# Kernel tuning notes

Hardware: AMD Instinct MI355X
Metric: run time of the kernel (lower is better)

The kernel has to match this reference:

```python
import jax, jax.numpy as jnp
import numpy as np

N_NODES = 50000
N_EDGES = 800000
NUM_GRAPHS = 256
IN_FEAT = 64
REL_DIM = 32
HID = 128
NUM_RELS = 32
NUM_BASES = 8
NUM_LAYERS = 2


def setup_inputs() -> dict:
    key = jax.random.key(0)
    ks = jax.random.split(key, 24)
    s = 0.05
    inp = {
        'feat': jax.random.normal(ks[0], (N_NODES, IN_FEAT), jnp.float32),
        'query_rel': jax.random.randint(ks[1], (N_NODES,), 0, NUM_RELS),
        'src': jax.random.randint(ks[2], (N_EDGES,), 0, N_NODES),
        'dst': jax.random.randint(ks[3], (N_EDGES,), 0, N_NODES),
        'etypes': jax.random.randint(ks[4], (N_EDGES,), 0, NUM_RELS),
        'graph_id': jnp.sort(jax.random.randint(ks[5], (N_NODES,), 0, NUM_GRAPHS)),
        # parameters
        'rel_emb': jax.random.normal(ks[6], (NUM_RELS, REL_DIM), jnp.float32) * s,
        'W_in': jax.random.normal(ks[7], (IN_FEAT + REL_DIM, HID), jnp.float32) * s,
        'b_in': jnp.zeros((HID,), jnp.float32),
        'V': jax.random.normal(ks[8], (NUM_LAYERS, NUM_BASES, HID, HID), jnp.float32) * s,
        'comp': jax.random.normal(ks[9], (NUM_LAYERS, NUM_RELS, NUM_BASES), jnp.float32) * s,
        'W_loop': jax.random.normal(ks[10], (NUM_LAYERS, HID, HID), jnp.float32) * s,
        'b_loop': jnp.zeros((NUM_LAYERS, HID), jnp.float32),
        'W_attn': jax.random.normal(ks[11], (HID + REL_DIM, HID), jnp.float32) * s,
        'b_attn': jnp.zeros((HID,), jnp.float32),
        'w_score_attn': jax.random.normal(ks[12], (HID,), jnp.float32) * s,
        'b_score_attn': jnp.zeros((), jnp.float32),
        'w_out': jax.random.normal(ks[13], (HID,), jnp.float32) * s,
        'b_out': jnp.zeros((), jnp.float32),
    }
    return inp


def _forward(feat, rel_emb, W_in, b_in, V, comp, W_loop, b_loop,
             W_attn, b_attn, w_score_attn, b_score_attn, w_out, b_out,
             query_rel, src, dst, etypes, graph_id):
    N = feat.shape[0]
    er = rel_emb[query_rel]                                   # [N, R]
    h = jax.nn.relu(jnp.concatenate([feat, er], -1) @ W_in + b_in)  # [N, H]
    for l in range(NUM_LAYERS):
        # basis-first: transform all nodes by every basis, then gather+mix per edge
        t = jnp.einsum('nd,bde->bne', h, V[l])                # [B, N, H]
        c = comp[l][etypes]                                   # [E, B]
        msg = jnp.zeros((src.shape[0], HID), h.dtype)
        for b in range(NUM_BASES):                            # fixed small loop
            msg = msg + c[:, b:b + 1] * t[b][src]
        agg = jax.ops.segment_sum(msg, dst, num_segments=N)   # scatter-add to dst
        h = jax.nn.relu(agg + h @ W_loop[l] + b_loop[l])      # self-loop + bias
    # per-graph attention-weighted softmax pooling (segment softmax)
    a = jnp.tanh(jnp.concatenate([h, er], -1) @ W_attn + b_attn) @ w_score_attn + b_score_attn  # [N]
    m = jax.ops.segment_max(a, graph_id, num_segments=NUM_GRAPHS)
    ex = jnp.exp(a - m[graph_id])
    ssum = jax.ops.segment_sum(ex, graph_id, num_segments=NUM_GRAPHS)
    alpha = ex / ssum[graph_id]                               # [N]
    z = jax.ops.segment_sum(h * alpha[:, None], graph_id, num_segments=NUM_GRAPHS)  # [G, H]
    return z @ w_out + b_out                                  # [G]


def reference(feat, query_rel, src, dst, etypes, graph_id,
              rel_emb, W_in, b_in, V, comp, W_loop, b_loop,
              W_attn, b_attn, w_score_attn, b_score_attn, w_out, b_out):
    return _forward(feat, rel_emb, W_in, b_in, V, comp, W_loop, b_loop,
                    W_attn, b_attn, w_score_attn, b_score_attn, w_out, b_out,
                    query_rel, src, dst, etypes, graph_id)
```

## Files before the change

kernel.cpp:

```cpp
#include <hip/hip_runtime.h>
#include <hip/hip_fp16.h>

#define N_NODES   50000
#define N_EDGES   800000
#define NUM_GRAPHS 256
#define IN_FEAT   64
#define REL_DIM   32
#define HID       128
#define NUM_RELS  32
#define NUM_BASES 8
#define NUM_LAYERS 2

#define NBUCK 196
#define PBLK  512
#define CHUNK 1563
#define OFFN  (NBUCK * PBLK)
#define SC2_BLKS (OFFN / 256)

typedef __attribute__((ext_vector_type(8))) _Float16 f16x8;
typedef __attribute__((ext_vector_type(4))) float f32x4;
typedef __attribute__((ext_vector_type(2))) float f32x2;

__device__ __forceinline__ void gld_lds16(void* lds, const void* g) {
    __builtin_amdgcn_global_load_lds(
        (const __attribute__((address_space(1))) unsigned int*)g,
        (__attribute__((address_space(3))) unsigned int*)lds, 16, 0, 0);
}

__global__ void __launch_bounds__(256) k_bhist(const int* __restrict__ dst,
                                               int* __restrict__ off) {
    __shared__ int hist[NBUCK];
    int t = threadIdx.x;
    if (t < NBUCK) hist[t] = 0;
    __syncthreads();
    int base = blockIdx.x * CHUNK;
    for (int i = t; i < CHUNK; i += 256) {
        int e = base + i;
        if (e < N_EDGES) atomicAdd(&hist[dst[e] >> 8], 1);
    }
    __syncthreads();
    if (t < NBUCK) off[t * PBLK + blockIdx.x] = hist[t];
}

__global__ void __launch_bounds__(256) k_scan2_a(int* __restrict__ off,
                                                 int* __restrict__ bsum) {
    __shared__ int s[256];
    int t = threadIdx.x;
    int idx = blockIdx.x * 256 + t;
    int v = off[idx];
    s[t] = v;
    __syncthreads();
    for (int o = 1; o < 256; o <<= 1) {
        int u = (t >= o) ? s[t - o] : 0;
        __syncthreads();
        s[t] += u;
        __syncthreads();
    }
    off[idx] = s[t] - v;
    if (t == 255) bsum[blockIdx.x] = s[255];
}

__global__ void __launch_bounds__(512) k_scan2_b(int* __restrict__ bsum,
                                                 int* __restrict__ boff) {
    __shared__ int s[512];
    int t = threadIdx.x;
    int v = (t < SC2_BLKS) ? bsum[t] : 0;
    s[t] = v;
    __syncthreads();
    for (int o = 1; o < 512; o <<= 1) {
        int u = (t >= o) ? s[t - o] : 0;
        __syncthreads();
        s[t] += u;
        __syncthreads();
    }
    if (t < SC2_BLKS) boff[t] = s[t] - v;
}

__global__ void __launch_bounds__(256) k_scan2_c(int* __restrict__ off,
                                                 const int* __restrict__ boff) {
    int idx = blockIdx.x * 256 + threadIdx.x;
    off[idx] += boff[blockIdx.x];
}

__global__ void __launch_bounds__(256) k_bscatter(
    const int* __restrict__ src, const int* __restrict__ dst,
    const int* __restrict__ ety, const int* __restrict__ off,
    int* __restrict__ tmp) {
    __shared__ int cur[NBUCK];
    int t = threadIdx.x;
    if (t < NBUCK) cur[t] = off[t * PBLK + blockIdx.x];
    __syncthreads();
    int base = blockIdx.x * CHUNK;
    for (int i = t; i < CHUNK; i += 256) {
        int e = base + i;
        if (e < N_EDGES) {
            int d = dst[e];
            int pos = atomicAdd(&cur[d >> 8], 1);
            tmp[pos] = ((d & 255) << 21) | (src[e] << 5) | ety[e];
        }
    }
}

__global__ void __launch_bounds__(256) k_bsort(
    const int* __restrict__ off, const int* __restrict__ tmp,
    int* __restrict__ edge_p, int* __restrict__ row_start) {
    int b = blockIdx.x, t = threadIdx.x;
    int eb = off[b * PBLK];
    int ee = (b == NBUCK - 1) ? N_EDGES : off[(b + 1) * PBLK];
    __shared__ int cnt[256];
    __shared__ int cur[256];
    cnt[t] = 0;
    __syncthreads();
    for (int i = eb + t; i < ee; i += 256)
        atomicAdd(&cnt[(tmp[i] >> 21) & 255], 1);
    __syncthreads();
    int v = cnt[t];
    __shared__ int s[256];
    s[t] = v;
    __syncthreads();
    for (int o = 1; o < 256; o <<= 1) {
        int u = (t >= o) ? s[t - o] : 0;
        __syncthreads();
        s[t] += u;
        __syncthreads();
    }
    int excl = s[t] - v;
    cur[t] = eb + excl;
    int node = b * 256 + t;
    if (node < N_NODES) row_start[node] = eb + excl;
    if (b == NBUCK - 1 && t == 0) row_start[N_NODES] = N_EDGES;
    __syncthreads();
    for (int i = eb + t; i < ee; i += 256) {
        int x = tmp[i];
        int pos = atomicAdd(&cur[(x >> 21) & 255], 1);
        edge_p[pos] = x & 0x1FFFFF;
    }
}

__global__ void __launch_bounds__(128) k_input(
    const float* __restrict__ feat, const int* __restrict__ qrel,
    const float* __restrict__ rel_emb, const float* __restrict__ Wi,
    const float* __restrict__ bi, unsigned short* __restrict__ h16,
    float* __restrict__ er) {
    int n0 = blockIdx.x * 16;
    int j = threadIdx.x;
    int u = j >> 3, q = j & 7;
    __shared__ float xT[96][16];
    {
        const float4* f4 = (const float4*)(feat + (size_t)(n0 + u) * IN_FEAT);
        float4 a = f4[q], b = f4[q + 8];
        xT[4 * q + 0][u] = a.x; xT[4 * q + 1][u] = a.y;
        xT[4 * q + 2][u] = a.z; xT[4 * q + 3][u] = a.w;
        xT[32 + 4 * q + 0][u] = b.x; xT[32 + 4 * q + 1][u] = b.y;
        xT[32 + 4 * q + 2][u] = b.z; xT[32 + 4 * q + 3][u] = b.w;
        int qr = qrel[n0 + u];
        float4 e4 = ((const float4*)(rel_emb + (size_t)qr * REL_DIM))[q];
        xT[64 + 4 * q + 0][u] = e4.x; xT[64 + 4 * q + 1][u] = e4.y;
        xT[64 + 4 * q + 2][u] = e4.z; xT[64 + 4 * q + 3][u] = e4.w;
        ((float4*)(er + (size_t)(n0 + u) * REL_DIM))[q] = e4;
    }
    __syncthreads();
    float bj = bi[j];
    float acc[16];
#pragma unroll
    for (int k = 0; k < 16; k++) acc[k] = bj;
    for (int d = 0; d < 96; d++) {
        float w = Wi[d * HID + j];
        float4 x0 = *(const float4*)&xT[d][0];
        float4 x1 = *(const float4*)&xT[d][4];
        float4 x2 = *(const float4*)&xT[d][8];
        float4 x3 = *(const float4*)&xT[d][12];
        acc[0]  = fmaf(x0.x, w, acc[0]);  acc[1]  = fmaf(x0.y, w, acc[1]);
        acc[2]  = fmaf(x0.z, w, acc[2]);  acc[3]  = fmaf(x0.w, w, acc[3]);
        acc[4]  = fmaf(x1.x, w, acc[4]);  acc[5]  = fmaf(x1.y, w, acc[5]);
        acc[6]  = fmaf(x1.z, w, acc[6]);  acc[7]  = fmaf(x1.w, w, acc[7]);
        acc[8]  = fmaf(x2.x, w, acc[8]);  acc[9]  = fmaf(x2.y, w, acc[9]);
        acc[10] = fmaf(x2.z, w, acc[10]); acc[11] = fmaf(x2.w, w, acc[11]);
        acc[12] = fmaf(x3.x, w, acc[12]); acc[13] = fmaf(x3.y, w, acc[13]);
        acc[14] = fmaf(x3.z, w, acc[14]); acc[15] = fmaf(x3.w, w, acc[15]);
    }
#pragma unroll
    for (int k = 0; k < 16; k++) {
        float v = fmaxf(acc[k], 0.f);
        __half hv = __float2half(v);
        h16[(size_t)(n0 + k) * HID + j] = __builtin_bit_cast(unsigned short, hv);
    }
}

__global__ void __launch_bounds__(256) k_mix2(
    const unsigned short* __restrict__ h16, const float* __restrict__ comp_l,
    const int* __restrict__ row_start, const int* __restrict__ edge_p,
    unsigned short* __restrict__ Gf, int c0, int nc) {
    __shared__ f32x2 cs2[NUM_RELS * NUM_BASES];
    if (threadIdx.x < NUM_RELS * NUM_BASES) {
        float c = comp_l[threadIdx.x];
        cs2[threadIdx.x] = (f32x2){c, c};
    }
    __syncthreads();
    int wave = threadIdx.x >> 6, lane = threadIdx.x & 63;
    int n = c0 + blockIdx.x * 4 + wave;
    if (n >= c0 + nc) return;
    int e0 = row_start[n], e1 = row_start[n + 1];
    f32x2 acc[NUM_BASES] = {};
    int e = e0;
    for (; e + 8 <= e1; e += 8) {
        int p0 = edge_p[e],     p1 = edge_p[e + 1], p2 = edge_p[e + 2], p3 = edge_p[e + 3];
        int p4 = edge_p[e + 4], p5 = edge_p[e + 5], p6 = edge_p[e + 6], p7 = edge_p[e + 7];
        unsigned u0 = ((const unsigned*)(h16 + (size_t)(p0 >> 5) * HID))[lane];
        unsigned u1 = ((const unsigned*)(h16 + (size_t)(p1 >> 5) * HID))[lane];
        unsigned u2 = ((const unsigned*)(h16 + (size_t)(p2 >> 5) * HID))[lane];
        unsigned u3 = ((const unsigned*)(h16 + (size_t)(p3 >> 5) * HID))[lane];
        unsigned u4 = ((const unsigned*)(h16 + (size_t)(p4 >> 5) * HID))[lane];
        unsigned u5 = ((const unsigned*)(h16 + (size_t)(p5 >> 5) * HID))[lane];
        unsigned u6 = ((const unsigned*)(h16 + (size_t)(p6 >> 5) * HID))[lane];
        unsigned u7 = ((const unsigned*)(h16 + (size_t)(p7 >> 5) * HID))[lane];
        const f32x2* c0p = &cs2[(p0 & 31) * NUM_BASES];
        const f32x2* c1p = &cs2[(p1 & 31) * NUM_BASES];
        const f32x2* c2p = &cs2[(p2 & 31) * NUM_BASES];
        const f32x2* c3p = &cs2[(p3 & 31) * NUM_BASES];
        const f32x2* c4p = &cs2[(p4 & 31) * NUM_BASES];
        const f32x2* c5p = &cs2[(p5 & 31) * NUM_BASES];
        const f32x2* c6p = &cs2[(p6 & 31) * NUM_BASES];
        const f32x2* c7p = &cs2[(p7 & 31) * NUM_BASES];
        float2 t0 = __half22float2(__builtin_bit_cast(__half2, u0));
        float2 t1 = __half22float2(__builtin_bit_cast(__half2, u1));
        float2 t2 = __half22float2(__builtin_bit_cast(__half2, u2));
        float2 t3 = __half22float2(__builtin_bit_cast(__half2, u3));
        float2 t4 = __half22float2(__builtin_bit_cast(__half2, u4));
        float2 t5 = __half22float2(__builtin_bit_cast(__half2, u5));
        float2 t6 = __half22float2(__builtin_bit_cast(__half2, u6));
        float2 t7 = __half22float2(__builtin_bit_cast(__half2, u7));
        f32x2 v0 = {t0.x, t0.y}, v1 = {t1.x, t1.y}, v2 = {t2.x, t2.y}, v3 = {t3.x, t3.y};
        f32x2 v4 = {t4.x, t4.y}, v5 = {t5.x, t5.y}, v6 = {t6.x, t6.y}, v7 = {t7.x, t7.y};
#pragma unroll
        for (int b = 0; b < NUM_BASES; b++) {
            acc[b] += c0p[b] * v0;
            acc[b] += c1p[b] * v1;
            acc[b] += c2p[b] * v2;
            acc[b] += c3p[b] * v3;
            acc[b] += c4p[b] * v4;
            acc[b] += c5p[b] * v5;
            acc[b] += c6p[b] * v6;
            acc[b] += c7p[b] * v7;
        }
    }
    for (; e < e1; e++) {
        int se = edge_p[e];
        const f32x2* cp = &cs2[(se & 31) * NUM_BASES];
        unsigned u = ((const unsigned*)(h16 + (size_t)(se >> 5) * HID))[lane];
        float2 tv = __half22float2(__builtin_bit_cast(__half2, u));
        f32x2 v = {tv.x, tv.y};
#pragma unroll
        for (int b = 0; b < NUM_BASES; b++) acc[b] += cp[b] * v;
    }
    size_t base = (size_t)(n - c0) * 1024 + 2 * lane;
#pragma unroll
    for (int b = 0; b < NUM_BASES; b++) {
        __half2 g2 = __floats2half2_rn(acc[b][0], acc[b][1]);
        *(unsigned*)&Gf[base + b * 128] = __builtin_bit_cast(unsigned, g2);
    }
}

__global__ void k_bfrag(const float* __restrict__ V, const float* __restrict__ W_loop,
                        unsigned short* __restrict__ Bf) {
    int idx = blockIdx.x * 256 + threadIdx.x;
    if (idx >= NUM_LAYERS * 36 * 8 * 64) return;
    int lane = idx & 63;
    int t = (idx >> 6) & 7;
    int s = (idx >> 9) % 36;
    int l = (idx >> 9) / 36;
    int col = t * 16 + (lane & 15);
    int kbase = s * 32 + (lane >> 4) * 8;
    unsigned short* o = Bf + (size_t)idx * 8;
#pragma unroll
    for (int j = 0; j < 8; j++) {
        int k = kbase + j;
        float f = (k < 1024) ? V[((size_t)l * 1024 + k) * HID + col]
                             : W_loop[((size_t)l * HID + (k - 1024)) * HID + col];
        __half hh = __float2half(f);
        o[j] = __builtin_bit_cast(unsigned short, hh);
    }
}

__global__ void __launch_bounds__(256) k_gemm9(
    const unsigned short* __restrict__ Gf, const unsigned short* __restrict__ h16,
    const unsigned short* __restrict__ Bf, const float* __restrict__ bl,
    unsigned short* __restrict__ out16, int c0, int nc) {
    __shared__ unsigned short smem[2][16][512];
    int lane = threadIdx.x & 63;
    int w = threadIdx.x >> 6;
    int rit = lane & 15, kg = lane >> 4;
    int r0 = blockIdx.x * 64;
    int sr0 = r0 + 0 * 16 + rit; if (sr0 >= nc) sr0 = nc - 1;
    int sr1 = r0 + 1 * 16 + rit; if (sr1 >= nc) sr1 = nc - 1;
    int sr2 = r0 + 2 * 16 + rit; if (sr2 >= nc) sr2 = nc - 1;
    int sr3 = r0 + 3 * 16 + rit; if (sr3 >= nc) sr3 = nc - 1;
    int koff = w * 32 + kg * 8;
    const unsigned short* gs0 = Gf + (size_t)sr0 * 1024 + koff;
    const unsigned short* gs1 = Gf + (size_t)sr1 * 1024 + koff;
    const unsigned short* gs2 = Gf + (size_t)sr2 * 1024 + koff;
    const unsigned short* gs3 = Gf + (size_t)sr3 * 1024 + koff;
    const f16x8* bb = (const f16x8*)Bf + (size_t)(2 * w) * 64 + lane;
    f32x4 acc[4][2] = {};

#define STAGE(BUF, STEP) {                                        \
        gld_lds16(&smem[BUF][w * 4 + 0][0], gs0 + (STEP) * 128);  \
        gld_lds16(&smem[BUF][w * 4 + 1][0], gs1 + (STEP) * 128);  \
        gld_lds16(&smem[BUF][w * 4 + 2][0], gs2 + (STEP) * 128);  \
        gld_lds16(&smem[BUF][w * 4 + 3][0], gs3 + (STEP) * 128); }
#define CSTEP(BUF, STEP) _Pragma("unroll")                                   \
    for (int s = 0; s < 4; s++) {                                            \
        const f16x8* bp = bb + (size_t)((STEP) * 4 + s) * 512;               \
        f16x8 bh0 = bp[0], bh1 = bp[64];                                     \
        _Pragma("unroll")                                                    \
        for (int i = 0; i < 4; i++) {                                        \
            f16x8 a = *(const f16x8*)&smem[BUF][s * 4 + i][lane * 8];        \
            acc[i][0] = __builtin_amdgcn_mfma_f32_16x16x32_f16(a, bh0, acc[i][0], 0, 0, 0); \
            acc[i][1] = __builtin_amdgcn_mfma_f32_16x16x32_f16(a, bh1, acc[i][1], 0, 0, 0); \
        }                                                                    \
    }

    STAGE(0, 0);
    for (int t = 0; t < 8; t++) {
        __syncthreads();
        if (t < 7) STAGE((t + 1) & 1, t + 1);
        CSTEP(t & 1, t);
    }
    {
        const unsigned short* hp0 = h16 + (size_t)(c0 + sr0) * HID + kg * 8;
        const unsigned short* hp1 = h16 + (size_t)(c0 + sr1) * HID + kg * 8;
        const unsigned short* hp2 = h16 + (size_t)(c0 + sr2) * HID + kg * 8;
        const unsigned short* hp3 = h16 + (size_t)(c0 + sr3) * HID + kg * 8;
#pragma unroll
        for (int s = 32; s < 36; s++) {
            int o = (s - 32) * 32;
            f16x8 a0 = *(const f16x8*)(hp0 + o);
            f16x8 a1 = *(const f16x8*)(hp1 + o);
            f16x8 a2 = *(const f16x8*)(hp2 + o);
            f16x8 a3 = *(const f16x8*)(hp3 + o);
            const f16x8* bp = bb + (size_t)s * 512;
            f16x8 bh0 = bp[0], bh1 = bp[64];
            acc[0][0] = __builtin_amdgcn_mfma_f32_16x16x32_f16(a0, bh0, acc[0][0], 0, 0, 0);
            acc[0][1] = __builtin_amdgcn_mfma_f32_16x16x32_f16(a0, bh1, acc[0][1], 0, 0, 0);
            acc[1][0] = __builtin_amdgcn_mfma_f32_16x16x32_f16(a1, bh0, acc[1][0], 0, 0, 0);
            acc[1][1] = __builtin_amdgcn_mfma_f32_16x16x32_f16(a1, bh1, acc[1][1], 0, 0, 0);
            acc[2][0] = __builtin_amdgcn_mfma_f32_16x16x32_f16(a2, bh0, acc[2][0], 0, 0, 0);
            acc[2][1] = __builtin_amdgcn_mfma_f32_16x16x32_f16(a2, bh1, acc[2][1], 0, 0, 0);
            acc[3][0] = __builtin_amdgcn_mfma_f32_16x16x32_f16(a3, bh0, acc[3][0], 0, 0, 0);
            acc[3][1] = __builtin_amdgcn_mfma_f32_16x16x32_f16(a3, bh1, acc[3][1], 0, 0, 0);
        }
    }
#undef STAGE
#undef CSTEP
    int col0 = 2 * w * 16 + rit;
    float b0 = bl[col0], b1 = bl[col0 + 16];
#pragma unroll
    for (int i = 0; i < 4; i++) {
        int rq = r0 + i * 16 + kg * 4;
#pragma unroll
        for (int q = 0; q < 4; q++) {
            int row = rq + q;
            if (row < nc) {
                float v0 = fmaxf(acc[i][0][q] + b0, 0.f);
                float v1 = fmaxf(acc[i][1][q] + b1, 0.f);
                size_t o = (size_t)(c0 + row) * HID;
                out16[o + col0] = __builtin_bit_cast(unsigned short, __float2half(v0));
                out16[o + col0 + 16] = __builtin_bit_cast(unsigned short, __float2half(v1));
            }
        }
    }
}

__global__ void __launch_bounds__(128) k_score(
    const unsigned short* __restrict__ h16, const float* __restrict__ er,
    const float* __restrict__ Wa, const float* __restrict__ ba,
    const float* __restrict__ wsc, const float* __restrict__ bsc,
    float* __restrict__ a) {
    int n0 = blockIdx.x * 16;
    int j = threadIdx.x;
    int u = j >> 3, q = j & 7;
    __shared__ float xT[160][16];
    {
        const uint2* h2 = (const uint2*)(h16 + (size_t)(n0 + u) * HID);
#pragma unroll
        for (int k = 0; k < 4; k++) {
            uint2 v = h2[q + 8 * k];
            float2 f01 = __half22float2(__builtin_bit_cast(__half2, v.x));
            float2 f23 = __half22float2(__builtin_bit_cast(__half2, v.y));
            xT[32 * k + 4 * q + 0][u] = f01.x; xT[32 * k + 4 * q + 1][u] = f01.y;
            xT[32 * k + 4 * q + 2][u] = f23.x; xT[32 * k + 4 * q + 3][u] = f23.y;
        }
        float4 e4 = ((const float4*)(er + (size_t)(n0 + u) * REL_DIM))[q];
        xT[128 + 4 * q + 0][u] = e4.x; xT[128 + 4 * q + 1][u] = e4.y;
        xT[128 + 4 * q + 2][u] = e4.z; xT[128 + 4 * q + 3][u] = e4.w;
    }
    __syncthreads();
    float bj = ba[j];
    float acc[16];
#pragma unroll
    for (int k = 0; k < 16; k++) acc[k] = bj;
    for (int d = 0; d < 160; d++) {
        float w = Wa[d * HID + j];
        float4 x0 = *(const float4*)&xT[d][0];
        float4 x1 = *(const float4*)&xT[d][4];
        float4 x2 = *(const float4*)&xT[d][8];
        float4 x3 = *(const float4*)&xT[d][12];
        acc[0]  = fmaf(x0.x, w, acc[0]);  acc[1]  = fmaf(x0.y, w, acc[1]);
        acc[2]  = fmaf(x0.z, w, acc[2]);  acc[3]  = fmaf(x0.w, w, acc[3]);
        acc[4]  = fmaf(x1.x, w, acc[4]);  acc[5]  = fmaf(x1.y, w, acc[5]);
        acc[6]  = fmaf(x1.z, w, acc[6]);  acc[7]  = fmaf(x1.w, w, acc[7]);
        acc[8]  = fmaf(x2.x, w, acc[8]);  acc[9]  = fmaf(x2.y, w, acc[9]);
        acc[10] = fmaf(x2.z, w, acc[10]); acc[11] = fmaf(x2.w, w, acc[11]);
        acc[12] = fmaf(x3.x, w, acc[12]); acc[13] = fmaf(x3.y, w, acc[13]);
        acc[14] = fmaf(x3.z, w, acc[14]); acc[15] = fmaf(x3.w, w, acc[15]);
    }
    __shared__ float red[16][128];
    float wj = wsc[j];
#pragma unroll
    for (int k = 0; k < 16; k++) red[k][j] = tanhf(acc[k]) * wj;
    __syncthreads();
    for (int s = 64; s > 0; s >>= 1) {
        if (j < s) {
#pragma unroll
            for (int k = 0; k < 16; k++) red[k][j] += red[k][j + s];
        }
        __syncthreads();
    }
    if (j < 16) a[n0 + j] = red[j][0] + bsc[0];
}

__global__ void k_starts(const int* __restrict__ gid, int* __restrict__ starts) {
    int g = threadIdx.x;
    int lo = 0, hi = N_NODES;
    while (lo < hi) {
        int mid = (lo + hi) >> 1;
        if (gid[mid] < g) lo = mid + 1; else hi = mid;
    }
    starts[g] = lo;
    if (g == 0) starts[NUM_GRAPHS] = N_NODES;
}

__global__ void __launch_bounds__(128) k_pool(
    const unsigned short* __restrict__ h16, const float* __restrict__ a,
    const int* __restrict__ starts, const float* __restrict__ wout,
    const float* __restrict__ bout, float* __restrict__ out) {
    int g = blockIdx.x, j = threadIdx.x;
    int s0 = starts[g], s1 = starts[g + 1];
    __shared__ float red[128];
    __shared__ float exb[128];
    if (s1 <= s0) { if (j == 0) out[g] = bout[0]; return; }
    float m = -3.4e38f;
    for (int i = s0 + j; i < s1; i += 128) m = fmaxf(m, a[i]);
    red[j] = m; __syncthreads();
    for (int s = 64; s > 0; s >>= 1) {
        if (j < s) red[j] = fmaxf(red[j], red[j + s]);
        __syncthreads();
    }
    m = red[0]; __syncthreads();
    float zj = 0.f, ss = 0.f;
    for (int base = s0; base < s1; base += 128) {
        int cnt = min(128, s1 - base);
        float ev = 0.f;
        if (j < cnt) ev = expf(a[base + j] - m);
        exb[j] = ev;
        ss += ev;
        __syncthreads();
        for (int k = 0; k < cnt; k++) {
            __half hv = __builtin_bit_cast(__half, h16[(size_t)(base + k) * HID + j]);
            zj = fmaf(exb[k], __half2float(hv), zj);
        }
        __syncthreads();
    }
    red[j] = ss; __syncthreads();
    for (int s = 64; s > 0; s >>= 1) {
        if (j < s) red[j] += red[j + s];
        __syncthreads();
    }
    ss = red[0]; __syncthreads();
    red[j] = (zj / ss) * wout[j]; __syncthreads();
    for (int s = 64; s > 0; s >>= 1) {
        if (j < s) red[j] += red[j + s];
        __syncthreads();
    }
    if (j == 0) out[g] = red[0] + bout[0];
}

extern "C" void kernel_launch(void* const* d_in, const int* in_sizes, int n_in,
                              void* d_out, int out_size, void* d_ws, size_t ws_size,
                              hipStream_t stream) {
    const float* feat    = (const float*)d_in[0];
    const int*   qrel    = (const int*)d_in[1];
    const int*   src     = (const int*)d_in[2];
    const int*   dst     = (const int*)d_in[3];
    const int*   ety     = (const int*)d_in[4];
    const int*   gid     = (const int*)d_in[5];
    const float* rel_emb = (const float*)d_in[6];
    const float* W_in    = (const float*)d_in[7];
    const float* b_in    = (const float*)d_in[8];
    const float* V       = (const float*)d_in[9];
    const float* comp    = (const float*)d_in[10];
    const float* W_loop  = (const float*)d_in[11];
    const float* b_loop  = (const float*)d_in[12];
    const float* W_attn  = (const float*)d_in[13];
    const float* b_attn  = (const float*)d_in[14];
    const float* w_sc    = (const float*)d_in[15];
    const float* b_sc    = (const float*)d_in[16];
    const float* w_out   = (const float*)d_in[17];
    const float* b_out   = (const float*)d_in[18];
    float* out = (float*)d_out;

    float* ws = (float*)d_ws;
    unsigned short* h16a = (unsigned short*)ws;
    unsigned short* h16b = h16a + (size_t)N_NODES * HID;
    float* er = (float*)(h16b + (size_t)N_NODES * HID);
    float* af = er + (size_t)N_NODES * REL_DIM;
    int* starts    = (int*)(af + N_NODES);
    int* row_start = starts + 260;
    int* off       = row_start + 50004;
    int* bsum      = off + OFFN;
    int* boff      = bsum + SC2_BLKS;
    int* tmp_e     = boff + SC2_BLKS;
    int* edge_p    = tmp_e + 800000;
    unsigned short* Bf = (unsigned short*)(edge_p + 800000);
    const size_t BF_USHORT = (size_t)NUM_LAYERS * 36 * 8 * 64 * 8;
    unsigned short* Gf = Bf + BF_USHORT;

    size_t used_floats = (size_t)((float*)Gf - ws);
    size_t total_floats = ws_size / sizeof(float);
    size_t avail = (total_floats > used_floats) ? (total_floats - used_floats) : 0;
    long long NC = (long long)(avail / 512);
    NC = (NC / 64) * 64;
    if (NC > 50048) NC = 50048;
    if (NC < 64) NC = 64;

    k_bhist<<<PBLK, 256, 0, stream>>>(dst, off);
    k_scan2_a<<<SC2_BLKS, 256, 0, stream>>>(off, bsum);
    k_scan2_b<<<1, 512, 0, stream>>>(bsum, boff);
    k_scan2_c<<<SC2_BLKS, 256, 0, stream>>>(off, boff);
    k_bscatter<<<PBLK, 256, 0, stream>>>(src, dst, ety, off, tmp_e);
    k_bsort<<<NBUCK, 256, 0, stream>>>(off, tmp_e, edge_p, row_start);
    k_bfrag<<<(NUM_LAYERS * 36 * 8 * 64 + 255) / 256, 256, 0, stream>>>(V, W_loop, Bf);
    k_input<<<N_NODES / 16, 128, 0, stream>>>(feat, qrel, rel_emb, W_in, b_in, h16a, er);

    unsigned short* h16cur = h16a;
    unsigned short* h16next = h16b;
    for (int l = 0; l < NUM_LAYERS; l++) {
        const float* comp_l = comp + (size_t)l * NUM_RELS * NUM_BASES;
        const unsigned short* Bfl = Bf + (size_t)l * 36 * 8 * 64 * 8;
        const float* bl = b_loop + (size_t)l * HID;
        for (int c0 = 0; c0 < N_NODES; c0 += (int)NC) {
            int nc = (int)((N_NODES - c0 < NC) ? (N_NODES - c0) : NC);
            k_mix2<<<(nc + 3) / 4, 256, 0, stream>>>(h16cur, comp_l, row_start, edge_p,
                                                     Gf, c0, nc);
            k_gemm9<<<(nc + 63) / 64, 256, 0, stream>>>(Gf, h16cur, Bfl, bl,
                                                        h16next, c0, nc);
        }
        unsigned short* tmp16 = h16cur; h16cur = h16next; h16next = tmp16;
    }

    k_score<<<N_NODES / 16, 128, 0, stream>>>(h16cur, er, W_attn, b_attn, w_sc, b_sc, af);
    k_starts<<<1, 256, 0, stream>>>(gid, starts);
    k_pool<<<NUM_GRAPHS, 128, 0, stream>>>(h16cur, af, starts, w_out, b_out, out);
}
```

Measured before the change: 312.5 us.

## Fuse edge aggregation and basis GEMM into one kernel via LDS staging

Replaces the separate per-chunk mix kernel and MFMA GEMM kernel with a single fused kernel. Each 512-thread block aggregates 32 destination nodes' basis-mixed messages into a swizzled LDS tile, then runs the MFMA GEMM against the fragment-packed weights plus the self-loop term. This removes the global round trip of the [N,1024] half-precision intermediate and the chunking logic. In exchange it uses 64 KB of LDS per block, which may reduce occupancy, and each block now has smaller GEMM tiles with less weight reuse.

Result: slower. 339.1 us (+8.5%).

```diff
diff --git a/kernel.cpp b/kernel.cpp
--- a/kernel.cpp
+++ b/kernel.cpp
@@ -20,12 +20,6 @@
 typedef __attribute__((ext_vector_type(8))) _Float16 f16x8;
 typedef __attribute__((ext_vector_type(4))) float f32x4;
 typedef __attribute__((ext_vector_type(2))) float f32x2;
-
-__device__ __forceinline__ void gld_lds16(void* lds, const void* g) {
-    __builtin_amdgcn_global_load_lds(
-        (const __attribute__((address_space(1))) unsigned int*)g,
-        (__attribute__((address_space(3))) unsigned int*)lds, 16, 0, 0);
-}
 
 __global__ void __launch_bounds__(256) k_bhist(const int* __restrict__ dst,
                                                int* __restrict__ off) {
@@ -187,77 +181,145 @@
     }
 }
 
-__global__ void __launch_bounds__(256) k_mix2(
+__global__ void __launch_bounds__(512) k_fused2(
     const unsigned short* __restrict__ h16, const float* __restrict__ comp_l,
     const int* __restrict__ row_start, const int* __restrict__ edge_p,
-    unsigned short* __restrict__ Gf, int c0, int nc) {
+    const unsigned short* __restrict__ Bf, const float* __restrict__ bl,
+    unsigned short* __restrict__ out16) {
+    __shared__ unsigned short Gt[64][512];
     __shared__ f32x2 cs2[NUM_RELS * NUM_BASES];
-    if (threadIdx.x < NUM_RELS * NUM_BASES) {
-        float c = comp_l[threadIdx.x];
-        cs2[threadIdx.x] = (f32x2){c, c};
-    }
-    __syncthreads();
-    int wave = threadIdx.x >> 6, lane = threadIdx.x & 63;
-    int n = c0 + blockIdx.x * 4 + wave;
-    if (n >= c0 + nc) return;
-    int e0 = row_start[n], e1 = row_start[n + 1];
-    f32x2 acc[NUM_BASES] = {};
-    int e = e0;
-    for (; e + 8 <= e1; e += 8) {
-        int p0 = edge_p[e],     p1 = edge_p[e + 1], p2 = edge_p[e + 2], p3 = edge_p[e + 3];
-        int p4 = edge_p[e + 4], p5 = edge_p[e + 5], p6 = edge_p[e + 6], p7 = edge_p[e + 7];
-        unsigned u0 = ((const unsigned*)(h16 + (size_t)(p0 >> 5) * HID))[lane];
-        unsigned u1 = ((const unsigned*)(h16 + (size_t)(p1 >> 5) * HID))[lane];
-        unsigned u2 = ((const unsigned*)(h16 + (size_t)(p2 >> 5) * HID))[lane];
-        unsigned u3 = ((const unsigned*)(h16 + (size_t)(p3 >> 5) * HID))[lane];
-        unsigned u4 = ((const unsigned*)(h16 + (size_t)(p4 >> 5) * HID))[lane];
-        unsigned u5 = ((const unsigned*)(h16 + (size_t)(p5 >> 5) * HID))[lane];
-        unsigned u6 = ((const unsigned*)(h16 + (size_t)(p6 >> 5) * HID))[lane];
-        unsigned u7 = ((const unsigned*)(h16 + (size_t)(p7 >> 5) * HID))[lane];
-        const f32x2* c0p = &cs2[(p0 & 31) * NUM_BASES];
-        const f32x2* c1p = &cs2[(p1 & 31) * NUM_BASES];
-        const f32x2* c2p = &cs2[(p2 & 31) * NUM_BASES];
-        const f32x2* c3p = &cs2[(p3 & 31) * NUM_BASES];
-        const f32x2* c4p = &cs2[(p4 & 31) * NUM_BASES];
-        const f32x2* c5p = &cs2[(p5 & 31) * NUM_BASES];
-        const f32x2* c6p = &cs2[(p6 & 31) * NUM_BASES];
-        const f32x2* c7p = &cs2[(p7 & 31) * NUM_BASES];
-        float2 t0 = __half22float2(__builtin_bit_cast(__half2, u0));
-        float2 t1 = __half22float2(__builtin_bit_cast(__half2, u1));
-        float2 t2 = __half22float2(__builtin_bit_cast(__half2, u2));
-        float2 t3 = __half22float2(__builtin_bit_cast(__half2, u3));
-        float2 t4 = __half22float2(__builtin_bit_cast(__half2, u4));
-        float2 t5 = __half22float2(__builtin_bit_cast(__half2, u5));
-        float2 t6 = __half22float2(__builtin_bit_cast(__half2, u6));
-        float2 t7 = __half22float2(__builtin_bit_cast(__half2, u7));
-        f32x2 v0 = {t0.x, t0.y}, v1 = {t1.x, t1.y}, v2 = {t2.x, t2.y}, v3 = {t3.x, t3.y};
-        f32x2 v4 = {t4.x, t4.y}, v5 = {t5.x, t5.y}, v6 = {t6.x, t6.y}, v7 = {t7.x, t7.y};
-#pragma unroll
-        for (int b = 0; b < NUM_BASES; b++) {
-            acc[b] += c0p[b] * v0;
-            acc[b] += c1p[b] * v1;
-            acc[b] += c2p[b] * v2;
-            acc[b] += c3p[b] * v3;
-            acc[b] += c4p[b] * v4;
-            acc[b] += c5p[b] * v5;
-            acc[b] += c6p[b] * v6;
-            acc[b] += c7p[b] * v7;
-        }
-    }
-    for (; e < e1; e++) {
-        int se = edge_p[e];
-        const f32x2* cp = &cs2[(se & 31) * NUM_BASES];
-        unsigned u = ((const unsigned*)(h16 + (size_t)(se >> 5) * HID))[lane];
-        float2 tv = __half22float2(__builtin_bit_cast(__half2, u));
-        f32x2 v = {tv.x, tv.y};
-#pragma unroll
-        for (int b = 0; b < NUM_BASES; b++) acc[b] += cp[b] * v;
-    }
-    size_t base = (size_t)(n - c0) * 1024 + 2 * lane;
-#pragma unroll
-    for (int b = 0; b < NUM_BASES; b++) {
-        __half2 g2 = __floats2half2_rn(acc[b][0], acc[b][1]);
-        *(unsigned*)&Gf[base + b * 128] = __builtin_bit_cast(unsigned, g2);
+    int tid = threadIdx.x;
+    int lane = tid & 63, w = tid >> 6;
+    if (tid < NUM_RELS * NUM_BASES) {
+        float c = comp_l[tid];
+        cs2[tid] = (f32x2){c, c};
+    }
+    __syncthreads();
+    int r0 = blockIdx.x * 32;
+
+    {
+        int qq = (lane >> 2) & 3;
+        int lo2 = lane & 3;
+        int sb = lane >> 4;
+#pragma unroll
+        for (int u = 0; u < 4; u++) {
+            int rloc = w * 4 + u;
+            int n = r0 + rloc;
+            f32x2 acc[NUM_BASES] = {};
+            if (n < N_NODES) {
+                int e0 = row_start[n], e1 = row_start[n + 1];
+                int e = e0;
+                for (; e + 8 <= e1; e += 8) {
+                    int p0 = edge_p[e],     p1 = edge_p[e + 1];
+                    int p2 = edge_p[e + 2], p3 = edge_p[e + 3];
+                    int p4 = edge_p[e + 4], p5 = edge_p[e + 5];
+                    int p6 = edge_p[e + 6], p7 = edge_p[e + 7];
+                    unsigned u0 = ((const unsigned*)(h16 + (size_t)(p0 >> 5) * HID))[lane];
+                    unsigned u1 = ((const unsigned*)(h16 + (size_t)(p1 >> 5) * HID))[lane];
+                    unsigned u2 = ((const unsigned*)(h16 + (size_t)(p2 >> 5) * HID))[lane];
+                    unsigned u3 = ((const unsigned*)(h16 + (size_t)(p3 >> 5) * HID))[lane];
+                    unsigned u4 = ((const unsigned*)(h16 + (size_t)(p4 >> 5) * HID))[lane];
+                    unsigned u5 = ((const unsigned*)(h16 + (size_t)(p5 >> 5) * HID))[lane];
+                    unsigned u6 = ((const unsigned*)(h16 + (size_t)(p6 >> 5) * HID))[lane];
+                    unsigned u7 = ((const unsigned*)(h16 + (size_t)(p7 >> 5) * HID))[lane];
+                    const f32x2* c0p = &cs2[(p0 & 31) * NUM_BASES];
+                    const f32x2* c1p = &cs2[(p1 & 31) * NUM_BASES];
+                    const f32x2* c2p = &cs2[(p2 & 31) * NUM_BASES];
+                    const f32x2* c3p = &cs2[(p3 & 31) * NUM_BASES];
+                    const f32x2* c4p = &cs2[(p4 & 31) * NUM_BASES];
+                    const f32x2* c5p = &cs2[(p5 & 31) * NUM_BASES];
+                    const f32x2* c6p = &cs2[(p6 & 31) * NUM_BASES];
+                    const f32x2* c7p = &cs2[(p7 & 31) * NUM_BASES];
+                    float2 t0 = __half22float2(__builtin_bit_cast(__half2, u0));
+                    float2 t1 = __half22float2(__builtin_bit_cast(__half2, u1));
+                    float2 t2 = __half22float2(__builtin_bit_cast(__half2, u2));
+                    float2 t3 = __half22float2(__builtin_bit_cast(__half2, u3));
+                    float2 t4 = __half22float2(__builtin_bit_cast(__half2, u4));
+                    float2 t5 = __half22float2(__builtin_bit_cast(__half2, u5));
+                    float2 t6 = __half22float2(__builtin_bit_cast(__half2, u6));
+                    float2 t7 = __half22float2(__builtin_bit_cast(__half2, u7));
+                    f32x2 v0 = {t0.x, t0.y}, v1 = {t1.x, t1.y};
+                    f32x2 v2 = {t2.x, t2.y}, v3 = {t3.x, t3.y};
+                    f32x2 v4 = {t4.x, t4.y}, v5 = {t5.x, t5.y};
+                    f32x2 v6 = {t6.x, t6.y}, v7 = {t7.x, t7.y};
+#pragma unroll
+                    for (int b = 0; b < NUM_BASES; b++) {
+                        acc[b] += c0p[b] * v0;
+                        acc[b] += c1p[b] * v1;
+                        acc[b] += c2p[b] * v2;
+                        acc[b] += c3p[b] * v3;
+                        acc[b] += c4p[b] * v4;
+                        acc[b] += c5p[b] * v5;
+                        acc[b] += c6p[b] * v6;
+                        acc[b] += c7p[b] * v7;
+                    }
+                }
+                for (; e < e1; e++) {
+                    int se = edge_p[e];
+                    const f32x2* cp = &cs2[(se & 31) * NUM_BASES];
+                    unsigned uu = ((const unsigned*)(h16 + (size_t)(se >> 5) * HID))[lane];
+                    float2 tv = __half22float2(__builtin_bit_cast(__half2, uu));
+                    f32x2 v = {tv.x, tv.y};
+#pragma unroll
+                    for (int b = 0; b < NUM_BASES; b++) acc[b] += cp[b] * v;
+                }
+            }
+            int slotp = ((rloc & 15) ^ qq) + 16 * qq;
+            int pos = slotp * 8 + lo2 * 2;
+            int Fbase = sb * 2 + (rloc >> 4);
+#pragma unroll
+            for (int b = 0; b < NUM_BASES; b++) {
+                __half2 g2 = __floats2half2_rn(acc[b][0], acc[b][1]);
+                *(ushort2*)&Gt[b * 8 + Fbase][pos] =
+                    __builtin_bit_cast(ushort2, g2);
+            }
+        }
+    }
+    __syncthreads();
+
+    int rit = lane & 15, kg = lane >> 4;
+    int slotr = (lane ^ ((lane >> 4) & 3)) * 8;
+    const f16x8* bb = (const f16x8*)Bf + (size_t)w * 64 + lane;
+    f32x4 acc0 = {}, acc1 = {};
+#pragma unroll 4
+    for (int s = 0; s < 32; s++) {
+        f16x8 bh = bb[(size_t)s * 512];
+        f16x8 a0 = *(const f16x8*)&Gt[s * 2 + 0][slotr];
+        f16x8 a1 = *(const f16x8*)&Gt[s * 2 + 1][slotr];
+        acc0 = __builtin_amdgcn_mfma_f32_16x16x32_f16(a0, bh, acc0, 0, 0, 0);
+        acc1 = __builtin_amdgcn_mfma_f32_16x16x32_f16(a1, bh, acc1, 0, 0, 0);
+    }
+    {
+        int rT0 = r0 + rit;      if (rT0 >= N_NODES) rT0 = N_NODES - 1;
+        int rT1 = r0 + 16 + rit; if (rT1 >= N_NODES) rT1 = N_NODES - 1;
+        const unsigned short* hp0 = h16 + (size_t)rT0 * HID + kg * 8;
+        const unsigned short* hp1 = h16 + (size_t)rT1 * HID + kg * 8;
+#pragma unroll
+        for (int s = 32; s < 36; s++) {
+            int o = (s - 32) * 32;
+            f16x8 a0 = *(const f16x8*)(hp0 + o);
+            f16x8 a1 = *(const f16x8*)(hp1 + o);
+            f16x8 bh = bb[(size_t)s * 512];
+            acc0 = __builtin_amdgcn_mfma_f32_16x16x32_f16(a0, bh, acc0, 0, 0, 0);
+            acc1 = __builtin_amdgcn_mfma_f32_16x16x32_f16(a1, bh, acc1, 0, 0, 0);
+        }
+    }
+    int col = w * 16 + rit;
+    float bc = bl[col];
+#pragma unroll
+    for (int q = 0; q < 4; q++) {
+        int rA = r0 + kg * 4 + q;
+        if (rA < N_NODES) {
+            float v = fmaxf(acc0[q] + bc, 0.f);
+            out16[(size_t)rA * HID + col] =
+                __builtin_bit_cast(unsigned short, __float2half(v));
+        }
+        int rB = rA + 16;
+        if (rB < N_NODES) {
+            float v = fmaxf(acc1[q] + bc, 0.f);
+            out16[(size_t)rB * HID + col] =
+                __builtin_bit_cast(unsigned short, __float2half(v));
+        }
     }
 }
 
@@ -279,95 +341,6 @@
                              : W_loop[((size_t)l * HID + (k - 1024)) * HID + col];
         __half hh = __float2half(f);
         o[j] = __builtin_bit_cast(unsigned short, hh);
-    }
-}
-
-__global__ void __launch_bounds__(256) k_gemm9(
-    const unsigned short* __restrict__ Gf, const unsigned short* __restrict__ h16,
-    const unsigned short* __restrict__ Bf, const float* __restrict__ bl,
-    unsigned short* __restrict__ out16, int c0, int nc) {
-    __shared__ unsigned short smem[2][16][512];
-    int lane = threadIdx.x & 63;
-    int w = threadIdx.x >> 6;
-    int rit = lane & 15, kg = lane >> 4;
-    int r0 = blockIdx.x * 64;
-    int sr0 = r0 + 0 * 16 + rit; if (sr0 >= nc) sr0 = nc - 1;
-    int sr1 = r0 + 1 * 16 + rit; if (sr1 >= nc) sr1 = nc - 1;
-    int sr2 = r0 + 2 * 16 + rit; if (sr2 >= nc) sr2 = nc - 1;
-    int sr3 = r0 + 3 * 16 + rit; if (sr3 >= nc) sr3 = nc - 1;
-    int koff = w * 32 + kg * 8;
-    const unsigned short* gs0 = Gf + (size_t)sr0 * 1024 + koff;
-    const unsigned short* gs1 = Gf + (size_t)sr1 * 1024 + koff;
-    const unsigned short* gs2 = Gf + (size_t)sr2 * 1024 + koff;
-    const unsigned short* gs3 = Gf + (size_t)sr3 * 1024 + koff;
-    const f16x8* bb = (const f16x8*)Bf + (size_t)(2 * w) * 64 + lane;
-    f32x4 acc[4][2] = {};
-
-#define STAGE(BUF, STEP) {                                        \
-        gld_lds16(&smem[BUF][w * 4 + 0][0], gs0 + (STEP) * 128);  \
-        gld_lds16(&smem[BUF][w * 4 + 1][0], gs1 + (STEP) * 128);  \
-        gld_lds16(&smem[BUF][w * 4 + 2][0], gs2 + (STEP) * 128);  \
-        gld_lds16(&smem[BUF][w * 4 + 3][0], gs3 + (STEP) * 128); }
-#define CSTEP(BUF, STEP) _Pragma("unroll")                                   \
-    for (int s = 0; s < 4; s++) {                                            \
-        const f16x8* bp = bb + (size_t)((STEP) * 4 + s) * 512;               \
-        f16x8 bh0 = bp[0], bh1 = bp[64];                                     \
-        _Pragma("unroll")                                                    \
-        for (int i = 0; i < 4; i++) {                                        \
-            f16x8 a = *(const f16x8*)&smem[BUF][s * 4 + i][lane * 8];        \
-            acc[i][0] = __builtin_amdgcn_mfma_f32_16x16x32_f16(a, bh0, acc[i][0], 0, 0, 0); \
-            acc[i][1] = __builtin_amdgcn_mfma_f32_16x16x32_f16(a, bh1, acc[i][1], 0, 0, 0); \
-        }                                                                    \
-    }
-
-    STAGE(0, 0);
-    for (int t = 0; t < 8; t++) {
-        __syncthreads();
-        if (t < 7) STAGE((t + 1) & 1, t + 1);
-        CSTEP(t & 1, t);
-    }
-    {
-        const unsigned short* hp0 = h16 + (size_t)(c0 + sr0) * HID + kg * 8;
-        const unsigned short* hp1 = h16 + (size_t)(c0 + sr1) * HID + kg * 8;
-        const unsigned short* hp2 = h16 + (size_t)(c0 + sr2) * HID + kg * 8;
-        const unsigned short* hp3 = h16 + (size_t)(c0 + sr3) * HID + kg * 8;
-#pragma unroll
-        for (int s = 32; s < 36; s++) {
-            int o = (s - 32) * 32;
-            f16x8 a0 = *(const f16x8*)(hp0 + o);
-            f16x8 a1 = *(const f16x8*)(hp1 + o);
-            f16x8 a2 = *(const f16x8*)(hp2 + o);
-            f16x8 a3 = *(const f16x8*)(hp3 + o);
-            const f16x8* bp = bb + (size_t)s * 512;
-            f16x8 bh0 = bp[0], bh1 = bp[64];
-            acc[0][0] = __builtin_amdgcn_mfma_f32_16x16x32_f16(a0, bh0, acc[0][0], 0, 0, 0);
-            acc[0][1] = __builtin_amdgcn_mfma_f32_16x16x32_f16(a0, bh1, acc[0][1], 0, 0, 0);
-            acc[1][0] = __builtin_amdgcn_mfma_f32_16x16x32_f16(a1, bh0, acc[1][0], 0, 0, 0);
-            acc[1][1] = __builtin_amdgcn_mfma_f32_16x16x32_f16(a1, bh1, acc[1][1], 0, 0, 0);
-            acc[2][0] = __builtin_amdgcn_mfma_f32_16x16x32_f16(a2, bh0, acc[2][0], 0, 0, 0);
-            acc[2][1] = __builtin_amdgcn_mfma_f32_16x16x32_f16(a2, bh1, acc[2][1], 0, 0, 0);
-            acc[3][0] = __builtin_amdgcn_mfma_f32_16x16x32_f16(a3, bh0, acc[3][0], 0, 0, 0);
-            acc[3][1] = __builtin_amdgcn_mfma_f32_16x16x32_f16(a3, bh1, acc[3][1], 0, 0, 0);
-        }
-    }
-#undef STAGE
-#undef CSTEP
-    int col0 = 2 * w * 16 + rit;
-    float b0 = bl[col0], b1 = bl[col0 + 16];
-#pragma unroll
-    for (int i = 0; i < 4; i++) {
-        int rq = r0 + i * 16 + kg * 4;
-#pragma unroll
-        for (int q = 0; q < 4; q++) {
-            int row = rq + q;
-            if (row < nc) {
-                float v0 = fmaxf(acc[i][0][q] + b0, 0.f);
-                float v1 = fmaxf(acc[i][1][q] + b1, 0.f);
-                size_t o = (size_t)(c0 + row) * HID;
-                out16[o + col0] = __builtin_bit_cast(unsigned short, __float2half(v0));
-                out16[o + col0 + 16] = __builtin_bit_cast(unsigned short, __float2half(v1));
-            }
-        }
     }
 }
 
@@ -522,16 +495,6 @@
     int* tmp_e     = boff + SC2_BLKS;
     int* edge_p    = tmp_e + 800000;
     unsigned short* Bf = (unsigned short*)(edge_p + 800000);
-    const size_t BF_USHORT = (size_t)NUM_LAYERS * 36 * 8 * 64 * 8;
-    unsigned short* Gf = Bf + BF_USHORT;
-
-    size_t used_floats = (size_t)((float*)Gf - ws);
-    size_t total_floats = ws_size / sizeof(float);
-    size_t avail = (total_floats > used_floats) ? (total_floats - used_floats) : 0;
-    long long NC = (long long)(avail / 512);
-    NC = (NC / 64) * 64;
-    if (NC > 50048) NC = 50048;
-    if (NC < 64) NC = 64;
 
     k_bhist<<<PBLK, 256, 0, stream>>>(dst, off);
     k_scan2_a<<<SC2_BLKS, 256, 0, stream>>>(off, bsum);
@@ -548,13 +511,8 @@
         const float* comp_l = comp + (size_t)l * NUM_RELS * NUM_BASES;
         const unsigned short* Bfl = Bf + (size_t)l * 36 * 8 * 64 * 8;
         const float* bl = b_loop + (size_t)l * HID;
-        for (int c0 = 0; c0 < N_NODES; c0 += (int)NC) {
-            int nc = (int)((N_NODES - c0 < NC) ? (N_NODES - c0) : NC);
-            k_mix2<<<(nc + 3) / 4, 256, 0, stream>>>(h16cur, comp_l, row_start, edge_p,
-                                                     Gf, c0, nc);
-            k_gemm9<<<(nc + 63) / 64, 256, 0, stream>>>(Gf, h16cur, Bfl, bl,
-                                                        h16next, c0, nc);
-        }
+        k_fused2<<<(N_NODES + 31) / 32, 512, 0, stream>>>(h16cur, comp_l, row_start,
+                                                          edge_p, Bfl, bl, h16next);
         unsigned short* tmp16 = h16cur; h16cur = h16next; h16next = tmp16;
     }
 
```

## Store mixed features in MFMA fragment order and load directly in GEMM

Applied to the files above, without the earlier changes.

k_mix2 now writes the per-node basis-mixed features in a tiled layout of 16-row tiles that matches the MFMA A-operand fragment order. k_gemm10 can then read A fragments straight from global memory with vector loads, and the LDS double-buffer staging and its syncthreads are gone. The chunking of nodes by workspace size is also removed, so each layer runs as one mix launch and one GEMM launch over all nodes. The trade-off is that the GEMM no longer stages through LDS, so it relies on direct global loads being well coalesced. The code also assumes the workspace can hold the full tiled buffer for all nodes (NTILES is defined but never used).

Measured after the change: 385.5 us. 1.23x slower.

```diff
diff --git a/kernel.cpp b/kernel.cpp
--- a/kernel.cpp
+++ b/kernel.cpp
@@ -16,16 +16,11 @@
 #define CHUNK 1563
 #define OFFN  (NBUCK * PBLK)
 #define SC2_BLKS (OFFN / 256)
+#define NTILES 3128
 
 typedef __attribute__((ext_vector_type(8))) _Float16 f16x8;
 typedef __attribute__((ext_vector_type(4))) float f32x4;
 typedef __attribute__((ext_vector_type(2))) float f32x2;
-
-__device__ __forceinline__ void gld_lds16(void* lds, const void* g) {
-    __builtin_amdgcn_global_load_lds(
-        (const __attribute__((address_space(1))) unsigned int*)g,
-        (__attribute__((address_space(3))) unsigned int*)lds, 16, 0, 0);
-}
 
 __global__ void __launch_bounds__(256) k_bhist(const int* __restrict__ dst,
                                                int* __restrict__ off) {
@@ -190,7 +185,7 @@
 __global__ void __launch_bounds__(256) k_mix2(
     const unsigned short* __restrict__ h16, const float* __restrict__ comp_l,
     const int* __restrict__ row_start, const int* __restrict__ edge_p,
-    unsigned short* __restrict__ Gf, int c0, int nc) {
+    unsigned short* __restrict__ Gf) {
     __shared__ f32x2 cs2[NUM_RELS * NUM_BASES];
     if (threadIdx.x < NUM_RELS * NUM_BASES) {
         float c = comp_l[threadIdx.x];
@@ -198,8 +193,8 @@
     }
     __syncthreads();
     int wave = threadIdx.x >> 6, lane = threadIdx.x & 63;
-    int n = c0 + blockIdx.x * 4 + wave;
-    if (n >= c0 + nc) return;
+    int n = blockIdx.x * 4 + wave;
+    if (n >= N_NODES) return;
     int e0 = row_start[n], e1 = row_start[n + 1];
     f32x2 acc[NUM_BASES] = {};
     int e = e0;
@@ -253,11 +248,16 @@
 #pragma unroll
         for (int b = 0; b < NUM_BASES; b++) acc[b] += cp[b] * v;
     }
-    size_t base = (size_t)(n - c0) * 1024 + 2 * lane;
+    int sgrp = lane >> 4;
+    int qq = (lane >> 2) & 3;
+    int jj = 2 * (lane & 3);
+    unsigned short* base = Gf + (size_t)(n >> 4) * 16384
+                              + ((n & 15) + 16 * qq) * 8 + jj;
 #pragma unroll
     for (int b = 0; b < NUM_BASES; b++) {
         __half2 g2 = __floats2half2_rn(acc[b][0], acc[b][1]);
-        *(unsigned*)&Gf[base + b * 128] = __builtin_bit_cast(unsigned, g2);
+        *(ushort2*)(base + (size_t)(b * 4 + sgrp) * 512) =
+            __builtin_bit_cast(ushort2, g2);
     }
 }
 
@@ -282,55 +282,46 @@
     }
 }
 
-__global__ void __launch_bounds__(256) k_gemm9(
+__global__ void __launch_bounds__(256) k_gemm10(
     const unsigned short* __restrict__ Gf, const unsigned short* __restrict__ h16,
     const unsigned short* __restrict__ Bf, const float* __restrict__ bl,
-    unsigned short* __restrict__ out16, int c0, int nc) {
-    __shared__ unsigned short smem[2][16][512];
+    unsigned short* __restrict__ out16) {
     int lane = threadIdx.x & 63;
     int w = threadIdx.x >> 6;
     int rit = lane & 15, kg = lane >> 4;
     int r0 = blockIdx.x * 64;
-    int sr0 = r0 + 0 * 16 + rit; if (sr0 >= nc) sr0 = nc - 1;
-    int sr1 = r0 + 1 * 16 + rit; if (sr1 >= nc) sr1 = nc - 1;
-    int sr2 = r0 + 2 * 16 + rit; if (sr2 >= nc) sr2 = nc - 1;
-    int sr3 = r0 + 3 * 16 + rit; if (sr3 >= nc) sr3 = nc - 1;
-    int koff = w * 32 + kg * 8;
-    const unsigned short* gs0 = Gf + (size_t)sr0 * 1024 + koff;
-    const unsigned short* gs1 = Gf + (size_t)sr1 * 1024 + koff;
-    const unsigned short* gs2 = Gf + (size_t)sr2 * 1024 + koff;
-    const unsigned short* gs3 = Gf + (size_t)sr3 * 1024 + koff;
+    const unsigned short* ga0 = Gf + (size_t)(r0 / 16 + 0) * 16384 + lane * 8;
+    const unsigned short* ga1 = Gf + (size_t)(r0 / 16 + 1) * 16384 + lane * 8;
+    const unsigned short* ga2 = Gf + (size_t)(r0 / 16 + 2) * 16384 + lane * 8;
+    const unsigned short* ga3 = Gf + (size_t)(r0 / 16 + 3) * 16384 + lane * 8;
     const f16x8* bb = (const f16x8*)Bf + (size_t)(2 * w) * 64 + lane;
     f32x4 acc[4][2] = {};
-
-#define STAGE(BUF, STEP) {                                        \
-        gld_lds16(&smem[BUF][w * 4 + 0][0], gs0 + (STEP) * 128);  \
-        gld_lds16(&smem[BUF][w * 4 + 1][0], gs1 + (STEP) * 128);  \
-        gld_lds16(&smem[BUF][w * 4 + 2][0], gs2 + (STEP) * 128);  \
-        gld_lds16(&smem[BUF][w * 4 + 3][0], gs3 + (STEP) * 128); }
-#define CSTEP(BUF, STEP) _Pragma("unroll")                                   \
-    for (int s = 0; s < 4; s++) {                                            \
-        const f16x8* bp = bb + (size_t)((STEP) * 4 + s) * 512;               \
-        f16x8 bh0 = bp[0], bh1 = bp[64];                                     \
-        _Pragma("unroll")                                                    \
-        for (int i = 0; i < 4; i++) {                                        \
-            f16x8 a = *(const f16x8*)&smem[BUF][s * 4 + i][lane * 8];        \
-            acc[i][0] = __builtin_amdgcn_mfma_f32_16x16x32_f16(a, bh0, acc[i][0], 0, 0, 0); \
-            acc[i][1] = __builtin_amdgcn_mfma_f32_16x16x32_f16(a, bh1, acc[i][1], 0, 0, 0); \
-        }                                                                    \
-    }
-
-    STAGE(0, 0);
-    for (int t = 0; t < 8; t++) {
-        __syncthreads();
-        if (t < 7) STAGE((t + 1) & 1, t + 1);
-        CSTEP(t & 1, t);
+#pragma unroll 8
+    for (int s = 0; s < 32; s++) {
+        f16x8 bh0 = bb[(size_t)s * 512];
+        f16x8 bh1 = bb[(size_t)s * 512 + 64];
+        f16x8 a0 = *(const f16x8*)(ga0 + s * 512);
+        f16x8 a1 = *(const f16x8*)(ga1 + s * 512);
+        f16x8 a2 = *(const f16x8*)(ga2 + s * 512);
+        f16x8 a3 = *(const f16x8*)(ga3 + s * 512);
+        acc[0][0] = __builtin_amdgcn_mfma_f32_16x16x32_f16(a0, bh0, acc[0][0], 0, 0, 0);
+        acc[0][1] = __builtin_amdgcn_mfma_f32_16x16x32_f16(a0, bh1, acc[0][1], 0, 0, 0);
+        acc[1][0] = __builtin_amdgcn_mfma_f32_16x16x32_f16(a1, bh0, acc[1][0], 0, 0, 0);
+        acc[1][1] = __builtin_amdgcn_mfma_f32_16x16x32_f16(a1, bh1, acc[1][1], 0, 0, 0);
+        acc[2][0] = __builtin_amdgcn_mfma_f32_16x16x32_f16(a2, bh0, acc[2][0], 0, 0, 0);
+        acc[2][1] = __builtin_amdgcn_mfma_f32_16x16x32_f16(a2, bh1, acc[2][1], 0, 0, 0);
+        acc[3][0] = __builtin_amdgcn_mfma_f32_16x16x32_f16(a3, bh0, acc[3][0], 0, 0, 0);
+        acc[3][1] = __builtin_amdgcn_mfma_f32_16x16x32_f16(a3, bh1, acc[3][1], 0, 0, 0);
     }
     {
-        const unsigned short* hp0 = h16 + (size_t)(c0 + sr0) * HID + kg * 8;
-        const unsigned short* hp1 = h16 + (size_t)(c0 + sr1) * HID + kg * 8;
-        const unsigned short* hp2 = h16 + (size_t)(c0 + sr2) * HID + kg * 8;
-        const unsigned short* hp3 = h16 + (size_t)(c0 + sr3) * HID + kg * 8;
+        int s0r = r0 + 0 * 16 + rit; if (s0r >= N_NODES) s0r = N_NODES - 1;
+        int s1r = r0 + 1 * 16 + rit; if (s1r >= N_NODES) s1r = N_NODES - 1;
+        int s2r = r0 + 2 * 16 + rit; if (s2r >= N_NODES) s2r = N_NODES - 1;
+        int s3r = r0 + 3 * 16 + rit; if (s3r >= N_NODES) s3r = N_NODES - 1;
+        const unsigned short* hp0 = h16 + (size_t)s0r * HID + kg * 8;
+        const unsigned short* hp1 = h16 + (size_t)s1r * HID + kg * 8;
+        const unsigned short* hp2 = h16 + (size_t)s2r * HID + kg * 8;
+        const unsigned short* hp3 = h16 + (size_t)s3r * HID + kg * 8;
 #pragma unroll
         for (int s = 32; s < 36; s++) {
             int o = (s - 32) * 32;
@@ -338,8 +329,8 @@
             f16x8 a1 = *(const f16x8*)(hp1 + o);
             f16x8 a2 = *(const f16x8*)(hp2 + o);
             f16x8 a3 = *(const f16x8*)(hp3 + o);
-            const f16x8* bp = bb + (size_t)s * 512;
-            f16x8 bh0 = bp[0], bh1 = bp[64];
+            f16x8 bh0 = bb[(size_t)s * 512];
+            f16x8 bh1 = bb[(size_t)s * 512 + 64];
             acc[0][0] = __builtin_amdgcn_mfma_f32_16x16x32_f16(a0, bh0, acc[0][0], 0, 0, 0);
             acc[0][1] = __builtin_amdgcn_mfma_f32_16x16x32_f16(a0, bh1, acc[0][1], 0, 0, 0);
             acc[1][0] = __builtin_amdgcn_mfma_f32_16x16x32_f16(a1, bh0, acc[1][0], 0, 0, 0);
@@ -350,8 +341,6 @@
             acc[3][1] = __builtin_amdgcn_mfma_f32_16x16x32_f16(a3, bh1, acc[3][1], 0, 0, 0);
         }
     }
-#undef STAGE
-#undef CSTEP
     int col0 = 2 * w * 16 + rit;
     float b0 = bl[col0], b1 = bl[col0 + 16];
 #pragma unroll
@@ -360,10 +349,10 @@
 #pragma unroll
         for (int q = 0; q < 4; q++) {
             int row = rq + q;
-            if (row < nc) {
+            if (row < N_NODES) {
                 float v0 = fmaxf(acc[i][0][q] + b0, 0.f);
                 float v1 = fmaxf(acc[i][1][q] + b1, 0.f);
-                size_t o = (size_t)(c0 + row) * HID;
+                size_t o = (size_t)row * HID;
                 out16[o + col0] = __builtin_bit_cast(unsigned short, __float2half(v0));
                 out16[o + col0 + 16] = __builtin_bit_cast(unsigned short, __float2half(v1));
             }
@@ -525,14 +514,6 @@
     const size_t BF_USHORT = (size_t)NUM_LAYERS * 36 * 8 * 64 * 8;
     unsigned short* Gf = Bf + BF_USHORT;
 
-    size_t used_floats = (size_t)((float*)Gf - ws);
-    size_t total_floats = ws_size / sizeof(float);
-    size_t avail = (total_floats > used_floats) ? (total_floats - used_floats) : 0;
-    long long NC = (long long)(avail / 512);
-    NC = (NC / 64) * 64;
-    if (NC > 50048) NC = 50048;
-    if (NC < 64) NC = 64;
-
     k_bhist<<<PBLK, 256, 0, stream>>>(dst, off);
     k_scan2_a<<<SC2_BLKS, 256, 0, stream>>>(off, bsum);
     k_scan2_b<<<1, 512, 0, stream>>>(bsum, boff);
@@ -548,13 +529,9 @@
         const float* comp_l = comp + (size_t)l * NUM_RELS * NUM_BASES;
         const unsigned short* Bfl = Bf + (size_t)l * 36 * 8 * 64 * 8;
         const float* bl = b_loop + (size_t)l * HID;
-        for (int c0 = 0; c0 < N_NODES; c0 += (int)NC) {
-            int nc = (int)((N_NODES - c0 < NC) ? (N_NODES - c0) : NC);
-            k_mix2<<<(nc + 3) / 4, 256, 0, stream>>>(h16cur, comp_l, row_start, edge_p,
-                                                     Gf, c0, nc);
-            k_gemm9<<<(nc + 63) / 64, 256, 0, stream>>>(Gf, h16cur, Bfl, bl,
-                                                        h16next, c0, nc);
-        }
+        k_mix2<<<(N_NODES + 3) / 4, 256, 0, stream>>>(h16cur, comp_l, row_start,
+                                                      edge_p, Gf);
+        k_gemm10<<<(N_NODES + 63) / 64, 256, 0, stream>>>(Gf, h16cur, Bfl, bl, h16next);
         unsigned short* tmp16 = h16cur; h16cur = h16next; h16next = tmp16;
     }
 
```
